# Optimization experiments

Measured on AMD Instinct MI355X. Metric: run time of the kernel, lower is better.

Reference implementation:

```python
import jax, jax.numpy as jnp
import numpy as np

K = 3          # kernel_size per pseudo-coordinate dim
DIM = 3        # edge_attr dimensionality
M = K ** DIM   # total number of spline kernel weight matrices


def spline_conv(x, src, dst, pseudo, W, Wr, b):
    """Degree-1 open B-spline conv (torch_geometric SplineConv, aggr='mean').
    x: (N, C_in), pseudo: (E, DIM) in [0,1], W: (M, C_in, C_out), Wr: (C_in, C_out), b: (C_out,).
    """
    N, C_in = x.shape
    pos = pseudo * (K - 1)                      # (E, DIM) in [0, K-1]
    i0 = jnp.clip(jnp.floor(pos), 0, K - 2)     # lower knot index per dim
    frac = pos - i0                             # (E, DIM) linear basis fraction
    i0 = i0.astype(jnp.int32)
    strides = jnp.array([1, K, K * K], dtype=jnp.int32)
    xj = x[src]                                 # (E, C_in) irregular gather
    # accumulate basis-weighted neighbor features per (dst node, kernel index)
    acc = jnp.zeros((N * M, C_in), dtype=x.dtype)
    for bits in range(2 ** DIM):                # 8 corners of the linear B-spline support
        off = jnp.array([(bits >> d) & 1 for d in range(DIM)], dtype=jnp.int32)
        w = jnp.prod(jnp.where(off == 1, frac, 1.0 - frac), axis=1)       # (E,)
        kidx = jnp.sum((i0 + off[None, :]) * strides[None, :], axis=1)    # (E,) flat kernel idx
        acc = acc.at[dst * M + kidx].add(w[:, None] * xj)                 # scatter-add
    out = jnp.einsum('nmi,mio->no', acc.reshape(N, M, C_in), W)
    deg = jnp.zeros((N,), x.dtype).at[dst].add(1.0)                        # in-degree
    out = out / jnp.maximum(deg, 1.0)[:, None]                             # mean aggregation
    return out + x @ Wr + b                                                # root weight + bias


def setup_inputs() -> dict:
    key = jax.random.key(0)
    ks = jax.random.split(key, 16)
    N, E = 50000, 800000
    dims = [3, 64, 64, 64]
    inp = {
        "x": jax.random.normal(ks[0], (N, 3), jnp.float32),
        "edge_index": jax.random.randint(ks[1], (2, E), 0, N),
        "edge_attr": jax.random.uniform(ks[2], (E, DIM), dtype=jnp.float32),
    }
    for l in range(3):
        ci, co = dims[l], dims[l + 1]
        inp[f"W{l}"] = jax.random.normal(ks[3 + 3 * l], (M, ci, co), jnp.float32) * (1.0 / np.sqrt(ci * M))
        inp[f"root{l}"] = jax.random.normal(ks[4 + 3 * l], (ci, co), jnp.float32) * (1.0 / np.sqrt(ci))
        inp[f"b{l}"] = jnp.zeros((co,), jnp.float32)
    return inp


def reference(x, edge_index, edge_attr, W0, root0, b0, W1, root1, b1, W2, root2, b2):
    src, dst = edge_index[0], edge_index[1]   # PyG flow: source_to_target
    h = x
    for W, Wr, b in ((W0, root0, b0), (W1, root1, b1), (W2, root2, b2)):
        h = jax.nn.relu(spline_conv(h, src, dst, edge_attr, W, Wr, b))
    return h
```

## Files before the change

### kernel.cpp

```cpp
#include <hip/hip_runtime.h>
#include <cstdint>


typedef __attribute__((ext_vector_type(8))) short short8;
typedef __attribute__((ext_vector_type(4))) float floatx4;

#define AS1 __attribute__((address_space(1)))
#define AS3 __attribute__((address_space(3)))

__device__ inline short f2bf(float f) {
    union { float f; unsigned u; } x; x.f = f;
    unsigned r = x.u + 0x7FFF + ((x.u >> 16) & 1);
    return (short)(r >> 16);
}

__device__ inline float bf2f(unsigned short u) {
    union { unsigned u; float f; } x;
    x.u = ((unsigned)u) << 16;
    return x.f;
}


__global__ void count_kernel(const int* __restrict__ ei, int* __restrict__ count, int E) {
    int e = blockIdx.x * blockDim.x + threadIdx.x;
    if (e < E) atomicAdd(&count[ei[E + e]], 1);
}

__global__ __launch_bounds__(1024) void scan_tile_kernel(const int* __restrict__ count,
                                                         int* __restrict__ row_ptr,
                                                         int* __restrict__ bsum, int N) {
    __shared__ int wsum[16];
    int tid = threadIdx.x, lane = tid & 63, wid = tid >> 6;
    int i = blockIdx.x * 1024 + tid;
    int v = (i < N) ? count[i] : 0;
    int incl = v;
#pragma unroll
    for (int off = 1; off < 64; off <<= 1) {
        int t = __shfl_up(incl, off, 64);
        if (lane >= off) incl += t;
    }
    if (lane == 63) wsum[wid] = incl;
    __syncthreads();
    if (tid < 16) {
        int w = wsum[tid];
#pragma unroll
        for (int off = 1; off < 16; off <<= 1) {
            int t = __shfl_up(w, off, 16);
            if ((tid & 15) >= off) w += t;
        }
        wsum[tid] = w;
    }
    __syncthreads();
    int waveoff = (wid > 0) ? wsum[wid - 1] : 0;
    if (i < N) row_ptr[i] = waveoff + incl - v;
    if (tid == 1023) bsum[blockIdx.x] = waveoff + incl;
}

__global__ __launch_bounds__(64) void scan_bsum_kernel(const int* __restrict__ bsum,
                                                       int* __restrict__ boff,
                                                       int* __restrict__ tot, int nb) {
    int tid = threadIdx.x;
    int v = (tid < nb) ? bsum[tid] : 0;
    int incl = v;
#pragma unroll
    for (int off = 1; off < 64; off <<= 1) {
        int t = __shfl_up(incl, off, 64);
        if (tid >= off) incl += t;
    }
    boff[tid] = incl - v;
    if (tid == 63) tot[0] = incl;
}

__global__ __launch_bounds__(1024) void scan_add_kernel(int* __restrict__ row_ptr,
                                                        const int* __restrict__ boff,
                                                        const int* __restrict__ tot,
                                                        int* __restrict__ cursor, int N) {
    int i = blockIdx.x * 1024 + threadIdx.x;
    if (i < N) {
        int r = row_ptr[i] + boff[blockIdx.x];
        row_ptr[i] = r;
        cursor[i] = r;
    }
    if (i == 0) row_ptr[N] = tot[0];
}

__global__ void basis_sort_kernel(const int* __restrict__ ei, const float* __restrict__ attr,
                                  const int* __restrict__ count, int* __restrict__ cursor,
                                  int* __restrict__ s_meta, float* __restrict__ s_w,
                                  unsigned short* __restrict__ s_w8, int E) {
    int e = blockIdx.x * blockDim.x + threadIdx.x;
    if (e >= E) return;
    int src = ei[e];
    int dst = ei[E + e];
    float f[3]; int i0[3];
#pragma unroll
    for (int d = 0; d < 3; d++) {
        float pos = attr[e * 3 + d] * 2.0f;
        float fl = floorf(pos);
        fl = fminf(fmaxf(fl, 0.0f), 1.0f);
        i0[d] = (int)fl;
        f[d] = pos - fl;
    }
    int base = i0[0] + 3 * i0[1] + 9 * i0[2];
    float invd = 1.0f / fmaxf((float)count[dst], 1.0f);
    int p = atomicAdd(&cursor[dst], 1);
    s_meta[p] = src | (base << 24) | (i0[0] << 28) | (i0[1] << 29) | (i0[2] << 30);
    float w[8];
    short8 pk8;
#pragma unroll
    for (int c = 0; c < 8; c++) {
        float ww = invd;
#pragma unroll
        for (int d = 0; d < 3; d++) {
            int off = (c >> d) & 1;
            ww *= off ? f[d] : (1.0f - f[d]);
        }
        w[c] = ww;
        pk8[c] = f2bf(ww);
    }
    floatx4 w03 = {w[0], w[1], w[2], w[3]};
    floatx4 w47 = {w[4], w[5], w[6], w[7]};
    *(floatx4*)(s_w + (size_t)p * 8) = w03;
    *(floatx4*)(s_w + (size_t)p * 8 + 4) = w47;
    *(short8*)(s_w8 + (size_t)p * 8) = pk8;
}

__global__ void build_wb2(const float* __restrict__ Wa, const float* __restrict__ Ra,
                          unsigned short* __restrict__ wba,
                          const float* __restrict__ Wb, const float* __restrict__ Rb,
                          unsigned short* __restrict__ wbb) {
    int idx0 = blockIdx.x * blockDim.x + threadIdx.x;
    int half = idx0 / (4 * 56 * 64);
    if (half >= 2) return;
    int idx = idx0 - half * (4 * 56 * 64);
    const float* W = half ? Wb : Wa;
    const float* Wr = half ? Rb : Ra;
    unsigned short* wb = half ? wbb : wba;
    int l = idx & 63;
    int c = (idx >> 6) % 56;
    int t = idx / (56 * 64);
    int q = l >> 4, o = t * 16 + (l & 15);
    short8 out;
#pragma unroll
    for (int j = 0; j < 8; j++) {
        int k = c * 32 + q * 8 + j;
        float v = (k < 1728) ? W[(size_t)k * 64 + o] : Wr[(size_t)(k - 1728) * 64 + o];
        out[j] = f2bf(v);
    }
    *(short8*)(wb + (size_t)idx * 8) = out;
}

__global__ __launch_bounds__(256) void layer0_kernel(
    const float* __restrict__ x, const float* __restrict__ W0,
    const float* __restrict__ Wr, const float* __restrict__ bias,
    const int* __restrict__ row_ptr, const int* __restrict__ s_meta,
    const float* __restrict__ s_w, unsigned short* __restrict__ h_out, int N) {
    constexpr int NPB = 32, KT = 84;
    __shared__ __align__(16) float acc[NPB * 2 * KT];
    int tid = threadIdx.x, lane = tid & 63, wv = tid >> 6;
    int n0 = blockIdx.x * NPB;
    for (int k = tid; k < NPB * 2 * KT; k += 256) acc[k] = 0.0f;
    __syncthreads();

    int d = lane >> 5, hl = lane & 31;
    int c = hl / 3, i = hl - c * 3;
    bool act = (hl < 24);
    int cc = act ? c : 0;
    int coff = (c & 1) + 3 * ((c >> 1) & 1) + 9 * (c >> 2);

    for (int g2 = 0; g2 < 8; g2++) {
        int g = wv * 8 + g2;
        int n = n0 + g;
        if (n >= N) continue;
        if (lane < 3) acc[(g * 2) * KT + 81 + lane] = x[(size_t)n * 3 + lane];
        int rs = row_ptr[n], re = row_ptr[n + 1];
        int npairs = (re - rs + 1) >> 1;
        float* accd = &acc[(g * 2 + d) * KT];
        for (int pb = 0; pb < npairs; pb += 4) {
            int metas[4]; float ws_[4], xs_[4];
#pragma unroll
            for (int j = 0; j < 4; j++) {
                int ej = rs + (pb + j) * 2 + d;
                bool v = (pb + j < npairs) && (ej < re);
                int ec = v ? ej : rs;
                metas[j] = s_meta[ec];
                float wv_ = s_w[(size_t)ec * 8 + cc];
                ws_[j] = v ? wv_ : 0.0f;
            }
#pragma unroll
            for (int j = 0; j < 4; j++)
                xs_[j] = x[(size_t)(metas[j] & 0xFFFFFF) * 3 + i];
#pragma unroll
            for (int j = 0; j < 4; j++) {
                int kidx = ((metas[j] >> 24) & 0xF) + coff;
                if (act) accd[kidx * 3 + i] += ws_[j] * xs_[j];
            }
        }
    }
    __syncthreads();

    int o = lane;
    float wreg[KT];
#pragma unroll
    for (int k = 0; k < KT; k++)
        wreg[k] = (k < 81) ? W0[k * 64 + o] : Wr[(k - 81) * 64 + o];
    float bv = bias[o];
    for (int g = wv; g < NPB; g += 4) {
        int n = n0 + g;
        if (n >= N) break;
        float s = bv;
#pragma unroll
        for (int k4 = 0; k4 < KT; k4 += 4) {
            floatx4 a0 = *(const floatx4*)&acc[(g * 2) * KT + k4];
            floatx4 a1 = *(const floatx4*)&acc[(g * 2 + 1) * KT + k4];
            s += (a0.x + a1.x) * wreg[k4] + (a0.y + a1.y) * wreg[k4 + 1]
               + (a0.z + a1.z) * wreg[k4 + 2] + (a0.w + a1.w) * wreg[k4 + 3];
        }
        h_out[(size_t)n * 64 + o] = (unsigned short)f2bf(fmaxf(s, 0.0f));
    }
}

template <bool OUTF32>
__global__ __launch_bounds__(512, 4) void layer64_kernel(
    const unsigned short* __restrict__ h_in, const unsigned short* __restrict__ wb,
    const float* __restrict__ bias, const int* __restrict__ row_ptr,
    const int* __restrict__ s_meta, const unsigned short* __restrict__ s_w8,
    void* __restrict__ h_out, int N) {
    constexpr int NPB = 8;
    constexpr int RGS = 2704;
    __shared__ __align__(16) unsigned short lds[NPB * RGS];
    int tid = threadIdx.x, lane = tid & 63;
    int wvu = __builtin_amdgcn_readfirstlane(tid >> 6);
    int n0 = blockIdx.x * NPB;
    int srow = lane & 15, sgrp = lane >> 4;

    unsigned short* reg = &lds[(size_t)wvu * RGS];
    unsigned short* featL = reg;
    unsigned short* w8SL = reg + 2048;
    int* metaL = (int*)(reg + 2560);

    {
        int n = n0 + wvu;
        if (n >= N) {
            for (int k = lane; k < 1792; k += 64) reg[k] = 0;
        } else {
            {
                short8 z = {0, 0, 0, 0, 0, 0, 0, 0};
#pragma unroll
                for (int s = 0; s < 4; s++)
                    *(short8*)(featL + lane * 8 + s * 512) = z;
            }
            int r0a = srow % 3, r1a = (srow / 3) % 3, r2a = srow / 9;
            int rb = srow + 16;
            int r0b = rb % 3, r1b = (rb / 3) % 3, r2b = rb / 9;
            bool rv1 = (srow < 11);

            floatx4 facc[2][4];
#pragma unroll
            for (int mt = 0; mt < 2; mt++)
#pragma unroll
                for (int nt = 0; nt < 4; nt++)
                    facc[mt][nt] = (floatx4){0.0f, 0.0f, 0.0f, 0.0f};

            int rs = row_ptr[n], re = row_ptr[n + 1];
            int deg = re - rs;
            for (int wbo = 0; wbo < deg; wbo += 64) {
                __builtin_amdgcn_global_load_lds(
                    (const AS1 unsigned int*)(s_meta + rs + wbo + lane),
                    (AS3 unsigned int*)metaL, 4, 0, 0);
                __builtin_amdgcn_global_load_lds(
                    (const AS1 unsigned int*)(s_w8 + (size_t)(rs + wbo + lane) * 8),
                    (AS3 unsigned int*)w8SL, 16, 0, 0);
                asm volatile("s_waitcnt vmcnt(0)" ::: "memory");
                int dw = deg - wbo;
                int vmax = (dw < 64 ? dw : 64) - 1;
                for (int ch2 = 0; ch2 < 2; ch2++) {
                    int cb = ch2 * 32;
                    if (cb >= dw) break;
                    int nsl = dw - cb; if (nsl > 32) nsl = 32;
                    int ngl = (nsl + 7) >> 3;
                    for (int i = 0; i < ngl; i++) {
                        int el = cb + i * 8 + (lane >> 3);
                        if (el > vmax) el = vmax;
                        int ms = metaL[el] & 0xFFFFFF;
                        int c3 = (lane & 7) ^ (i << 1);
                        const unsigned short* srcp = h_in + (size_t)ms * 64 + c3 * 8;
                        __builtin_amdgcn_global_load_lds(
                            (const AS1 unsigned int*)srcp,
                            (AS3 unsigned int*)(featL + i * 512), 16, 0, 0);
                    }
                    short8 af0, af1;
#pragma unroll
                    for (int j = 0; j < 8; j++) {
                        int ec = cb + 8 * sgrp + j;
                        bool ve = ec < dw;
                        int m = metaL[ec];
                        int d0 = (m >> 28) & 1, d1 = (m >> 29) & 1, d2 = (m >> 30) & 1;
                        {
                            int c0 = r0a - d0, c1 = r1a - d1, c2 = r2a - d2;
                            bool vc = (((c0 | c1 | c2) & ~1) == 0) && ve;
                            int ci = (c0 + (c1 << 1) + (c2 << 2)) & 7;
                            unsigned short wv_ = w8SL[ec * 8 + ci];
                            af0[j] = vc ? (short)wv_ : (short)0;
                        }
                        {
                            int c0 = r0b - d0, c1 = r1b - d1, c2 = r2b - d2;
                            bool vc = rv1 && (((c0 | c1 | c2) & ~1) == 0) && ve;
                            int ci = (c0 + (c1 << 1) + (c2 << 2)) & 7;
                            unsigned short wv_ = w8SL[ec * 8 + ci];
                            af1[j] = vc ? (short)wv_ : (short)0;
                        }
                    }
                    asm volatile("s_waitcnt vmcnt(0)" ::: "memory");
#pragma unroll
                    for (int nt = 0; nt < 4; nt++) {
                        short8 bn;
#pragma unroll
                        for (int jj = 0; jj < 8; jj++) {
                            int e = sgrp * 8 + jj;
                            int g = e * 8 + (((nt * 2) + (srow >> 3)) ^ (sgrp << 1));
                            bn[jj] = (short)featL[g * 8 + (srow & 7)];
                        }
                        facc[0][nt] = __builtin_amdgcn_mfma_f32_16x16x32_bf16(
                            af0, bn, facc[0][nt], 0, 0, 0);
                        facc[1][nt] = __builtin_amdgcn_mfma_f32_16x16x32_bf16(
                            af1, bn, facc[1][nt], 0, 0, 0);
                    }
                }
            }
#pragma unroll
            for (int mt = 0; mt < 2; mt++)
#pragma unroll
                for (int nt = 0; nt < 4; nt++)
#pragma unroll
                    for (int r = 0; r < 4; r++) {
                        int mrow = mt * 16 + sgrp * 4 + r;
                        if (mrow < 27)
                            reg[mrow * 64 + nt * 16 + srow] =
                                (unsigned short)f2bf(facc[mt][nt][r]);
                    }
            reg[1728 + lane] = h_in[(size_t)n * 64 + lane];
        }
    }
    __syncthreads();

    {
        floatx4 f0 = {0.0f, 0.0f, 0.0f, 0.0f};
        floatx4 f1 = {0.0f, 0.0f, 0.0f, 0.0f};
        if (wvu < 4) {
            int hf = wvu >> 1;
            int tp = wvu & 1;
            const unsigned short* ap = lds + (size_t)(lane & 7) * RGS + ((lane >> 4) * 8);
            const unsigned short* wbp0 = wb + ((size_t)((tp * 2) * 56) * 64 + lane) * 8;
            const unsigned short* wbp1 = wb + ((size_t)((tp * 2 + 1) * 56) * 64 + lane) * 8;
#pragma unroll
            for (int ci = 0; ci < 28; ci++) {
                int c = hf * 28 + ci;
                short8 af = *(const short8*)(ap + c * 32);
                short8 b0 = *(const short8*)(wbp0 + (size_t)c * 64 * 8);
                short8 b1 = *(const short8*)(wbp1 + (size_t)c * 64 * 8);
                f0 = __builtin_amdgcn_mfma_f32_16x16x32_bf16(af, b0, f0, 0, 0, 0);
                f1 = __builtin_amdgcn_mfma_f32_16x16x32_bf16(af, b1, f1, 0, 0, 0);
            }
        }
        __syncthreads();
        if (wvu < 4) {
            float* pfw = (float*)(lds + (size_t)wvu * RGS);
#pragma unroll
            for (int r = 0; r < 4; r++) {
                pfw[r * 64 + lane] = f0[r];
                pfw[256 + r * 64 + lane] = f1[r];
            }
        }
        __syncthreads();
        if (wvu < 4) {
            int t = wvu;
            int o = t * 16 + (lane & 15);
            float bv = bias[o];
            const float* pfA = (const float*)(lds + (size_t)(t >> 1) * RGS)
                             + (t & 1) * 256;
            const float* pfB = (const float*)(lds + (size_t)(2 + (t >> 1)) * RGS)
                             + (t & 1) * 256;
#pragma unroll
            for (int r = 0; r < 4; r++) {
                int m = (lane >> 4) * 4 + r;
                if (m < 8) {
                    int n = n0 + m;
                    if (n < N) {
                        float s = pfA[r * 64 + lane] + pfB[r * 64 + lane];
                        float val = fmaxf(s + bv, 0.0f);
                        if (OUTF32) {
                            ((float*)h_out)[(size_t)n * 64 + o] = val;
                        } else {
                            ((unsigned short*)h_out)[(size_t)n * 64 + o] =
                                (unsigned short)f2bf(val);
                        }
                    }
                }
            }
        }
    }
}

extern "C" void kernel_launch(void* const* d_in, const int* in_sizes, int n_in,
                              void* d_out, int out_size, void* d_ws, size_t ws_size,
                              hipStream_t stream) {
    (void)n_in; (void)out_size; (void)ws_size;
    const float* x    = (const float*)d_in[0];
    const int*   ei   = (const int*)d_in[1];
    const float* attr = (const float*)d_in[2];
    const float* W0 = (const float*)d_in[3];
    const float* R0 = (const float*)d_in[4];
    const float* B0 = (const float*)d_in[5];
    const float* W1 = (const float*)d_in[6];
    const float* R1 = (const float*)d_in[7];
    const float* B1 = (const float*)d_in[8];
    const float* W2 = (const float*)d_in[9];
    const float* R2 = (const float*)d_in[10];
    const float* B2 = (const float*)d_in[11];
    const int N = in_sizes[0] / 3;
    const int E = in_sizes[1] / 2;

    char* ws = (char*)d_ws;
    size_t off = 0;
    auto alloc = [&](size_t bytes) {
        size_t cur = off;
        off = (off + bytes + 255) & ~(size_t)255;
        return cur;
    };
    int* row_ptr = (int*)(ws + alloc((size_t)(N + 1) * 4));
    int* count   = (int*)(ws + alloc((size_t)N * 4));
    int* cursor  = (int*)(ws + alloc((size_t)N * 4));
    int* bsum    = (int*)(ws + alloc(64 * 4));
    int* boff    = (int*)(ws + alloc(64 * 4));
    int* tot     = (int*)(ws + alloc(4));
    int* s_meta  = (int*)(ws + alloc((size_t)E * 4));
    float* s_w   = (float*)(ws + alloc((size_t)E * 8 * 4));
    unsigned short* s_w8 = (unsigned short*)(ws + alloc((size_t)E * 8 * 2));
    unsigned short* h_a  = (unsigned short*)(ws + alloc((size_t)N * 64 * 2));
    unsigned short* h_b  = (unsigned short*)(ws + alloc((size_t)N * 64 * 2));
    unsigned short* wb1  = (unsigned short*)(ws + alloc((size_t)4 * 56 * 64 * 8 * 2));
    unsigned short* wb2  = (unsigned short*)(ws + alloc((size_t)4 * 56 * 64 * 8 * 2));

    int nb = (N + 1023) / 1024;

    hipMemsetAsync(count, 0, (size_t)N * 4, stream);
    count_kernel<<<(E + 255) / 256, 256, 0, stream>>>(ei, count, E);
    scan_tile_kernel<<<nb, 1024, 0, stream>>>(count, row_ptr, bsum, N);
    scan_bsum_kernel<<<1, 64, 0, stream>>>(bsum, boff, tot, nb);
    scan_add_kernel<<<nb, 1024, 0, stream>>>(row_ptr, boff, tot, cursor, N);
    basis_sort_kernel<<<(E + 255) / 256, 256, 0, stream>>>(ei, attr, count, cursor,
                                                           s_meta, s_w, s_w8, E);
    build_wb2<<<(2 * 4 * 56 * 64 + 255) / 256, 256, 0, stream>>>(W1, R1, wb1,
                                                                 W2, R2, wb2);

    layer0_kernel<<<(N + 31) / 32, 256, 0, stream>>>(x, W0, R0, B0, row_ptr,
                                                     s_meta, s_w, h_a, N);
    layer64_kernel<false><<<(N + 7) / 8, 512, 0, stream>>>(h_a, wb1, B1, row_ptr,
                                                           s_meta, s_w8, h_b, N);
    layer64_kernel<true><<<(N + 7) / 8, 512, 0, stream>>>(h_b, wb2, B2, row_ptr,
                                                          s_meta, s_w8, d_out, N);
}
```

Baseline: 430.9 us.

## Precompute dense 27-slot basis weight columns per edge for MFMA operand staging

The basis kernel now writes, for each sorted edge, a zero-padded 32-entry bf16 row with the 8 corner weights scattered into their kernel slots. This replaces the packed 8-weight array. The layer64 kernel stages these rows into LDS and reads the MFMA A-operand directly, removing the per-element corner index arithmetic and selects. The second half-chunk's rows are staged after the first half is consumed. In exchange, the per-edge weight storage and the global traffic grow fourfold (64 bytes instead of 16 per edge), and LDS use per wave grows, which may reduce occupancy.

```diff
diff --git a/kernel.cpp b/kernel.cpp
--- a/kernel.cpp
+++ b/kernel.cpp
@@ -87,7 +87,7 @@
 __global__ void basis_sort_kernel(const int* __restrict__ ei, const float* __restrict__ attr,
                                   const int* __restrict__ count, int* __restrict__ cursor,
                                   int* __restrict__ s_meta, float* __restrict__ s_w,
-                                  unsigned short* __restrict__ s_w8, int E) {
+                                  unsigned short* __restrict__ s_wcol, int E) {
     int e = blockIdx.x * blockDim.x + threadIdx.x;
     if (e >= E) return;
     int src = ei[e];
@@ -104,9 +104,8 @@
     int base = i0[0] + 3 * i0[1] + 9 * i0[2];
     float invd = 1.0f / fmaxf((float)count[dst], 1.0f);
     int p = atomicAdd(&cursor[dst], 1);
-    s_meta[p] = src | (base << 24) | (i0[0] << 28) | (i0[1] << 29) | (i0[2] << 30);
+    s_meta[p] = src | (base << 24);
     float w[8];
-    short8 pk8;
 #pragma unroll
     for (int c = 0; c < 8; c++) {
         float ww = invd;
@@ -116,13 +115,22 @@
             ww *= off ? f[d] : (1.0f - f[d]);
         }
         w[c] = ww;
-        pk8[c] = f2bf(ww);
     }
     floatx4 w03 = {w[0], w[1], w[2], w[3]};
     floatx4 w47 = {w[4], w[5], w[6], w[7]};
     *(floatx4*)(s_w + (size_t)p * 8) = w03;
     *(floatx4*)(s_w + (size_t)p * 8 + 4) = w47;
-    *(short8*)(s_w8 + (size_t)p * 8) = pk8;
+    unsigned short* wc = s_wcol + (size_t)p * 32;
+    short8 z8 = {0, 0, 0, 0, 0, 0, 0, 0};
+    *(short8*)(wc) = z8;
+    *(short8*)(wc + 8) = z8;
+    *(short8*)(wc + 16) = z8;
+    *(short8*)(wc + 24) = z8;
+#pragma unroll
+    for (int c = 0; c < 8; c++) {
+        int coff = (c & 1) + 3 * ((c >> 1) & 1) + 9 * (c >> 2);
+        wc[base + coff] = (unsigned short)f2bf(w[c]);
+    }
 }
 
 __global__ void build_wb2(const float* __restrict__ Wa, const float* __restrict__ Ra,
@@ -224,10 +232,10 @@
 __global__ __launch_bounds__(512, 4) void layer64_kernel(
     const unsigned short* __restrict__ h_in, const unsigned short* __restrict__ wb,
     const float* __restrict__ bias, const int* __restrict__ row_ptr,
-    const int* __restrict__ s_meta, const unsigned short* __restrict__ s_w8,
-    void* __restrict__ h_out, int N) {
+    const int* __restrict__ s_meta, const unsigned short* __restrict__ s_wcol,
+    const unsigned short* __restrict__ zpad, void* __restrict__ h_out, int N) {
     constexpr int NPB = 8;
-    constexpr int RGS = 2704;
+    constexpr int RGS = 3216;
     __shared__ __align__(16) unsigned short lds[NPB * RGS];
     int tid = threadIdx.x, lane = tid & 63;
     int wvu = __builtin_amdgcn_readfirstlane(tid >> 6);
@@ -236,8 +244,19 @@
 
     unsigned short* reg = &lds[(size_t)wvu * RGS];
     unsigned short* featL = reg;
-    unsigned short* w8SL = reg + 2048;
-    int* metaL = (int*)(reg + 2560);
+    unsigned short* wcolL = reg + 2048;
+    int* metaL = (int*)(reg + 3072);
+
+#define STAGE_WCOL(CB) do { \
+    _Pragma("unroll") for (int k = 0; k < 2; k++) { \
+        int el = (CB) + k * 16 + (lane >> 2); \
+        const unsigned short* srcp = (el < dw) \
+            ? s_wcol + (size_t)(rs + wbo + el) * 32 + (lane & 3) * 8 \
+            : zpad + (lane & 3) * 8; \
+        __builtin_amdgcn_global_load_lds((const AS1 unsigned int*)srcp, \
+            (AS3 unsigned int*)(wcolL + k * 512), 16, 0, 0); \
+    } \
+} while (0)
 
     {
         int n = n0 + wvu;
@@ -250,11 +269,6 @@
                 for (int s = 0; s < 4; s++)
                     *(short8*)(featL + lane * 8 + s * 512) = z;
             }
-            int r0a = srow % 3, r1a = (srow / 3) % 3, r2a = srow / 9;
-            int rb = srow + 16;
-            int r0b = rb % 3, r1b = (rb / 3) % 3, r2b = rb / 9;
-            bool rv1 = (srow < 11);
-
             floatx4 facc[2][4];
 #pragma unroll
             for (int mt = 0; mt < 2; mt++)
@@ -265,14 +279,12 @@
             int rs = row_ptr[n], re = row_ptr[n + 1];
             int deg = re - rs;
             for (int wbo = 0; wbo < deg; wbo += 64) {
+                int dw = deg - wbo;
                 __builtin_amdgcn_global_load_lds(
                     (const AS1 unsigned int*)(s_meta + rs + wbo + lane),
                     (AS3 unsigned int*)metaL, 4, 0, 0);
-                __builtin_amdgcn_global_load_lds(
-                    (const AS1 unsigned int*)(s_w8 + (size_t)(rs + wbo + lane) * 8),
-                    (AS3 unsigned int*)w8SL, 16, 0, 0);
+                STAGE_WCOL(0);
                 asm volatile("s_waitcnt vmcnt(0)" ::: "memory");
-                int dw = deg - wbo;
                 int vmax = (dw < 64 ? dw : 64) - 1;
                 for (int ch2 = 0; ch2 < 2; ch2++) {
                     int cb = ch2 * 32;
@@ -290,26 +302,18 @@
                             (AS3 unsigned int*)(featL + i * 512), 16, 0, 0);
                     }
                     short8 af0, af1;
-#pragma unroll
-                    for (int j = 0; j < 8; j++) {
-                        int ec = cb + 8 * sgrp + j;
-                        bool ve = ec < dw;
-                        int m = metaL[ec];
-                        int d0 = (m >> 28) & 1, d1 = (m >> 29) & 1, d2 = (m >> 30) & 1;
-                        {
-                            int c0 = r0a - d0, c1 = r1a - d1, c2 = r2a - d2;
-                            bool vc = (((c0 | c1 | c2) & ~1) == 0) && ve;
-                            int ci = (c0 + (c1 << 1) + (c2 << 2)) & 7;
-                            unsigned short wv_ = w8SL[ec * 8 + ci];
-                            af0[j] = vc ? (short)wv_ : (short)0;
+                    {
+                        const unsigned short* wrp = wcolL + (8 * sgrp) * 32 + srow;
+#pragma unroll
+                        for (int j = 0; j < 8; j++) {
+                            af0[j] = (short)wrp[j * 32];
+                            af1[j] = (short)wrp[j * 32 + 16];
                         }
-                        {
-                            int c0 = r0b - d0, c1 = r1b - d1, c2 = r2b - d2;
-                            bool vc = rv1 && (((c0 | c1 | c2) & ~1) == 0) && ve;
-                            int ci = (c0 + (c1 << 1) + (c2 << 2)) & 7;
-                            unsigned short wv_ = w8SL[ec * 8 + ci];
-                            af1[j] = vc ? (short)wv_ : (short)0;
-                        }
+                    }
+                    if (ch2 == 0 && dw > 32) {
+                        asm volatile("s_waitcnt lgkmcnt(0)" ::: "memory");
+                        __builtin_amdgcn_sched_barrier(0);
+                        STAGE_WCOL(32);
                     }
                     asm volatile("s_waitcnt vmcnt(0)" ::: "memory");
 #pragma unroll
@@ -342,6 +346,7 @@
             reg[1728 + lane] = h_in[(size_t)n * 64 + lane];
         }
     }
+#undef STAGE_WCOL
     __syncthreads();
 
     {
@@ -434,9 +439,10 @@
     int* bsum    = (int*)(ws + alloc(64 * 4));
     int* boff    = (int*)(ws + alloc(64 * 4));
     int* tot     = (int*)(ws + alloc(4));
+    unsigned short* zpad = (unsigned short*)(ws + alloc(256));
     int* s_meta  = (int*)(ws + alloc((size_t)E * 4));
     float* s_w   = (float*)(ws + alloc((size_t)E * 8 * 4));
-    unsigned short* s_w8 = (unsigned short*)(ws + alloc((size_t)E * 8 * 2));
+    unsigned short* s_wcol = (unsigned short*)(ws + alloc((size_t)E * 32 * 2));
     unsigned short* h_a  = (unsigned short*)(ws + alloc((size_t)N * 64 * 2));
     unsigned short* h_b  = (unsigned short*)(ws + alloc((size_t)N * 64 * 2));
     unsigned short* wb1  = (unsigned short*)(ws + alloc((size_t)4 * 56 * 64 * 8 * 2));
@@ -445,19 +451,20 @@
     int nb = (N + 1023) / 1024;
 
     hipMemsetAsync(count, 0, (size_t)N * 4, stream);
+    hipMemsetAsync(zpad, 0, 256, stream);
     count_kernel<<<(E + 255) / 256, 256, 0, stream>>>(ei, count, E);
     scan_tile_kernel<<<nb, 1024, 0, stream>>>(count, row_ptr, bsum, N);
     scan_bsum_kernel<<<1, 64, 0, stream>>>(bsum, boff, tot, nb);
     scan_add_kernel<<<nb, 1024, 0, stream>>>(row_ptr, boff, tot, cursor, N);
     basis_sort_kernel<<<(E + 255) / 256, 256, 0, stream>>>(ei, attr, count, cursor,
-                                                           s_meta, s_w, s_w8, E);
+                                                           s_meta, s_w, s_wcol, E);
     build_wb2<<<(2 * 4 * 56 * 64 + 255) / 256, 256, 0, stream>>>(W1, R1, wb1,
                                                                  W2, R2, wb2);
 
     layer0_kernel<<<(N + 31) / 32, 256, 0, stream>>>(x, W0, R0, B0, row_ptr,
                                                      s_meta, s_w, h_a, N);
     layer64_kernel<false><<<(N + 7) / 8, 512, 0, stream>>>(h_a, wb1, B1, row_ptr,
-                                                           s_meta, s_w8, h_b, N);
+                                                           s_meta, s_wcol, zpad, h_b, N);
     layer64_kernel<true><<<(N + 7) / 8, 512, 0, stream>>>(h_b, wb2, B2, row_ptr,
-                                                          s_meta, s_w8, d_out, N);
-}
+                                                          s_meta, s_wcol, zpad, d_out, N);
+}
```

Measured after the change: 394.5 us. 1.09x faster.
